# Optimization experiments

Hardware: AMD Instinct MI355X
Metric: run time of the kernel (lower is better)

## Reference

```python
import jax, jax.numpy as jnp
import numpy as np

B, S, D = 64, 2048, 512


def setup_inputs() -> dict:
    key = jax.random.key(0)
    k1, k2, k3, k4 = jax.random.split(key, 4)
    decoder_output = jax.random.normal(k1, (B, 1, D), dtype=jnp.float32)
    encoder_output = jax.random.normal(k2, (B, S, D), dtype=jnp.float32)
    # W_a_tanh: Dense(D) applied to concat([dec, enc]) of width 2D
    scale_w = 1.0 / np.sqrt(2 * D)
    W_t = jax.random.normal(k3, (2 * D, D), dtype=jnp.float32) * scale_w
    b_t = jnp.zeros((D,), dtype=jnp.float32)
    # v_a: Dense(1)
    v_a = jax.random.normal(k4, (D, 1), dtype=jnp.float32) * (1.0 / np.sqrt(D))
    b_v = jnp.zeros((1,), dtype=jnp.float32)
    return {
        "decoder_output": decoder_output,
        "encoder_output": encoder_output,
        "W_t": W_t,
        "b_t": b_t,
        "v_a": v_a,
        "b_v": b_v,
    }


def reference(decoder_output, encoder_output, W_t, b_t, v_a, b_v):
    # concat-variant Luong attention
    dec = jnp.broadcast_to(decoder_output, encoder_output.shape)       # [B,S,D]
    concated = jnp.concatenate((dec, encoder_output), axis=-1)          # [B,S,2D]
    hidden = jnp.tanh(jnp.einsum('bse,ed->bsd', concated, W_t) + b_t)   # [B,S,D]
    score = (jnp.einsum('bsd,do->bso', hidden, v_a) + b_v)              # [B,S,1]
    score = jnp.transpose(score, (0, 2, 1))                             # [B,1,S]
    alignment_vector = jax.nn.softmax(score, axis=2)                    # [B,1,S]
    context_vector = jnp.matmul(alignment_vector, encoder_output)       # [B,1,D]
    return (context_vector, alignment_vector)
```

## Files before the change

kernel.cpp:

```cpp
#include <hip/hip_runtime.h>
#include <hip/hip_bf16.h>

#define BB 64
#define SS 2048
#define DD 512
#define MM (BB * SS)

typedef __attribute__((ext_vector_type(8))) short bf16x8;
typedef __attribute__((ext_vector_type(4))) float f32x4;

__device__ __forceinline__ unsigned f2bf(float f) {
    unsigned u = __float_as_uint(f);
    u += 0x7FFFu + ((u >> 16) & 1u);
    return u >> 16;
}

__device__ __forceinline__ float fast_tanh(float x) {
    float ax = fabsf(x);
    float e = __expf(-2.0f * ax);
    float t = (1.0f - e) * __builtin_amdgcn_rcpf(1.0f + e);
    return x < 0.0f ? -t : t;
}

__global__ void prep_w(const float* __restrict__ W, short* __restrict__ Bt) {
    __shared__ float tile[64][65];
    int kt = blockIdx.x >> 3;
    int nt = blockIdx.x & 7;
    int t = threadIdx.x;
    int c = t & 63;
    int rbase = (t >> 6) * 16;
    #pragma unroll
    for (int i = 0; i < 16; ++i) {
        int r = rbase + i;
        tile[r][c] = W[(size_t)(512 + kt * 64 + r) * DD + nt * 64 + c];
    }
    __syncthreads();
    #pragma unroll
    for (int i = 0; i < 16; ++i) {
        int r = rbase + i;
        Bt[(size_t)(nt * 64 + r) * DD + kt * 64 + c] = (short)f2bf(tile[c][r]);
    }
}

__global__ void prep_p(const float* __restrict__ dec, const float* __restrict__ W,
                       const float* __restrict__ bt, float* __restrict__ p) {
    int b = blockIdx.x;
    int d = blockIdx.y * 256 + threadIdx.x;
    float acc = bt[d];
    const float* dv = dec + (size_t)b * DD;
    #pragma unroll 8
    for (int e = 0; e < DD; ++e)
        acc += dv[e] * W[(size_t)e * DD + d];
    p[(size_t)b * DD + d] = acc;
}

__global__ __launch_bounds__(256, 2)
void score_gemm(const float* __restrict__ enc,
                const short* __restrict__ Bt,
                const float* __restrict__ p,
                const float* __restrict__ va,
                float* __restrict__ score) {
    __shared__ short Alds[2][128 * 32];
    __shared__ short Blds[2][128 * 32];
    __shared__ float sp[4][64];

    const int tid  = threadIdx.x;
    const int wave = tid >> 6;
    const int lane = tid & 63;
    const int mblk = blockIdx.x >> 2;
    const int n0   = (blockIdx.x & 3) * 128;
    const int m0   = mblk * 128;

    const int wm = wave >> 1, wn = wave & 1;
    const int lm = lane & 15, lq = lane >> 4;

    f32x4 acc[4][4];
    #pragma unroll
    for (int i = 0; i < 4; ++i)
        #pragma unroll
        for (int j = 0; j < 4; ++j)
            acc[i][j] = (f32x4){0.f, 0.f, 0.f, 0.f};

    const int arow = tid >> 1;
    const int acol = (tid & 1) * 16;
    const float* aptr = enc + (size_t)(m0 + arow) * DD + acol;

    const short* bptr = Bt + (size_t)(n0 + wave * 32 + (lane >> 2)) * DD + (lane & 3) * 8;

    #pragma unroll
    for (int i = 0; i < 2; ++i)
        __builtin_amdgcn_global_load_lds(
            (const __attribute__((address_space(1))) void*)(bptr + (size_t)i * 16 * DD),
            (__attribute__((address_space(3))) void*)(&Blds[0][(wave * 32 + i * 16) * 32]),
            16, 0, 0);
    {
        f32x4 x0 = *(const f32x4*)(aptr);
        f32x4 x1 = *(const f32x4*)(aptr + 4);
        f32x4 x2 = *(const f32x4*)(aptr + 8);
        f32x4 x3 = *(const f32x4*)(aptr + 12);
        int4 p0, p1;
        p0.x = f2bf(x0.x) | (f2bf(x0.y) << 16);
        p0.y = f2bf(x0.z) | (f2bf(x0.w) << 16);
        p0.z = f2bf(x1.x) | (f2bf(x1.y) << 16);
        p0.w = f2bf(x1.z) | (f2bf(x1.w) << 16);
        p1.x = f2bf(x2.x) | (f2bf(x2.y) << 16);
        p1.y = f2bf(x2.z) | (f2bf(x2.w) << 16);
        p1.z = f2bf(x3.x) | (f2bf(x3.y) << 16);
        p1.w = f2bf(x3.z) | (f2bf(x3.w) << 16);
        *(int4*)(&Alds[0][arow * 32 + acol]) = p0;
        *(int4*)(&Alds[0][arow * 32 + acol + 8]) = p1;
    }
    __syncthreads();

    for (int kt = 0; kt < 16; ++kt) {
        const int c = kt & 1;
        const bool pf = kt < 15;
        f32x4 x0, x1, x2, x3;
        if (pf) {
            const int kn = (kt + 1) * 32;
            #pragma unroll
            for (int i = 0; i < 2; ++i)
                __builtin_amdgcn_global_load_lds(
                    (const __attribute__((address_space(1))) void*)(bptr + (size_t)i * 16 * DD + kn),
                    (__attribute__((address_space(3))) void*)(&Blds[1 - c][(wave * 32 + i * 16) * 32]),
                    16, 0, 0);
            x0 = *(const f32x4*)(aptr + kn);
            x1 = *(const f32x4*)(aptr + kn + 4);
            x2 = *(const f32x4*)(aptr + kn + 8);
            x3 = *(const f32x4*)(aptr + kn + 12);
        }
        bf16x8 af[4];
        #pragma unroll
        for (int mf = 0; mf < 4; ++mf)
            af[mf] = *(const bf16x8*)(&Alds[c][(wm * 64 + mf * 16 + lm) * 32 + lq * 8]);
        #pragma unroll
        for (int nf = 0; nf < 4; ++nf) {
            bf16x8 bfr = *(const bf16x8*)(&Blds[c][(wn * 64 + nf * 16 + lm) * 32 + lq * 8]);
            #pragma unroll
            for (int mf = 0; mf < 4; ++mf)
                acc[mf][nf] = __builtin_amdgcn_mfma_f32_16x16x32_bf16(af[mf], bfr, acc[mf][nf], 0, 0, 0);
        }
        if (pf) {
            int4 p0, p1;
            p0.x = f2bf(x0.x) | (f2bf(x0.y) << 16);
            p0.y = f2bf(x0.z) | (f2bf(x0.w) << 16);
            p0.z = f2bf(x1.x) | (f2bf(x1.y) << 16);
            p0.w = f2bf(x1.z) | (f2bf(x1.w) << 16);
            p1.x = f2bf(x2.x) | (f2bf(x2.y) << 16);
            p1.y = f2bf(x2.z) | (f2bf(x2.w) << 16);
            p1.z = f2bf(x3.x) | (f2bf(x3.y) << 16);
            p1.w = f2bf(x3.z) | (f2bf(x3.w) << 16);
            *(int4*)(&Alds[1 - c][arow * 32 + acol]) = p0;
            *(int4*)(&Alds[1 - c][arow * 32 + acol + 8]) = p1;
        }
        __syncthreads();
    }

    const int b = m0 >> 11;
    float rowsum[4][4];
    #pragma unroll
    for (int mf = 0; mf < 4; ++mf)
        #pragma unroll
        for (int r = 0; r < 4; ++r) rowsum[mf][r] = 0.f;

    #pragma unroll
    for (int nf = 0; nf < 4; ++nf) {
        int n = n0 + wn * 64 + nf * 16 + lm;
        float pv = p[(size_t)b * DD + n];
        float vv = va[n];
        #pragma unroll
        for (int mf = 0; mf < 4; ++mf)
            #pragma unroll
            for (int r = 0; r < 4; ++r)
                rowsum[mf][r] += fast_tanh(pv + acc[mf][nf][r]) * vv;
    }
    #pragma unroll
    for (int mf = 0; mf < 4; ++mf)
        #pragma unroll
        for (int r = 0; r < 4; ++r) {
            float s = rowsum[mf][r];
            s += __shfl_xor(s, 1);
            s += __shfl_xor(s, 2);
            s += __shfl_xor(s, 4);
            s += __shfl_xor(s, 8);
            rowsum[mf][r] = s;
        }
    if (lm == 0) {
        #pragma unroll
        for (int mf = 0; mf < 4; ++mf)
            #pragma unroll
            for (int r = 0; r < 4; ++r)
                sp[wave][mf * 16 + lq * 4 + r] = rowsum[mf][r];
    }
    __syncthreads();
    if (tid < 128) {
        int row = tid & 63, half = tid >> 6;
        float v = sp[half * 2][row] + sp[half * 2 + 1][row];
        atomicAdd(&score[(size_t)m0 + half * 64 + row], v);
    }
}

__global__ void softmax_k(const float* __restrict__ score, float* __restrict__ align) {
    __shared__ float red[256];
    int b = blockIdx.x, tid = threadIdx.x;
    const float* s = score + (size_t)b * SS;
    float vals[8];
    float mx = -1e30f;
    #pragma unroll
    for (int i = 0; i < 8; ++i) {
        vals[i] = s[i * 256 + tid];
        mx = fmaxf(mx, vals[i]);
    }
    red[tid] = mx; __syncthreads();
    for (int off = 128; off > 0; off >>= 1) {
        if (tid < off) red[tid] = fmaxf(red[tid], red[tid + off]);
        __syncthreads();
    }
    mx = red[0]; __syncthreads();
    float sum = 0.f;
    #pragma unroll
    for (int i = 0; i < 8; ++i) {
        vals[i] = __expf(vals[i] - mx);
        sum += vals[i];
    }
    red[tid] = sum; __syncthreads();
    for (int off = 128; off > 0; off >>= 1) {
        if (tid < off) red[tid] += red[tid + off];
        __syncthreads();
    }
    float inv = 1.0f / red[0];
    #pragma unroll
    for (int i = 0; i < 8; ++i)
        align[(size_t)b * SS + i * 256 + tid] = vals[i] * inv;
}

__global__ void context_k(const float* __restrict__ enc, const float* __restrict__ align,
                          float* __restrict__ ctx) {
    int bx = blockIdx.x;
    int b = bx >> 4, chunk = bx & 15;
    int tid = threadIdx.x;
    const float2* e2 = (const float2*)(enc + ((size_t)b * SS + chunk * 128) * DD);
    const float* a = align + (size_t)b * SS + chunk * 128;
    float2 acc = {0.f, 0.f};
    #pragma unroll 4
    for (int s = 0; s < 128; ++s) {
        float av = a[s];
        float2 e = e2[(size_t)s * 256 + tid];
        acc.x += av * e.x;
        acc.y += av * e.y;
    }
    atomicAdd(&ctx[(size_t)b * DD + tid * 2], acc.x);
    atomicAdd(&ctx[(size_t)b * DD + tid * 2 + 1], acc.y);
}

extern "C" void kernel_launch(void* const* d_in, const int* in_sizes, int n_in,
                              void* d_out, int out_size, void* d_ws, size_t ws_size,
                              hipStream_t stream) {
    const float* dec = (const float*)d_in[0];
    const float* enc = (const float*)d_in[1];
    const float* W   = (const float*)d_in[2];
    const float* bt  = (const float*)d_in[3];
    const float* va  = (const float*)d_in[4];

    float* out   = (float*)d_out;
    float* ctx   = out;
    float* align = out + BB * DD;

    char*  ws    = (char*)d_ws;
    short* Bt    = (short*)ws;
    float* p     = (float*)(ws + 512 * 512 * 2);
    float* score = (float*)(ws + 512 * 512 * 2 + BB * DD * 4);

    hipMemsetAsync(ctx, 0, BB * DD * sizeof(float), stream);
    hipMemsetAsync(score, 0, MM * sizeof(float), stream);
    prep_w<<<64, 256, 0, stream>>>(W, Bt);
    prep_p<<<dim3(BB, 2), 256, 0, stream>>>(dec, W, bt, p);
    score_gemm<<<MM / 32, 256, 0, stream>>>(enc, Bt, p, va, score);
    softmax_k<<<BB, 256, 0, stream>>>(score, align);
    context_k<<<BB * 16, 256, 0, stream>>>(enc, align, ctx);
}
```

Before: 538.5 us.

## Fuse score GEMM, local softmax and context into one flash-style kernel

Replaces the separate score GEMM, softmax and context kernels with one fused kernel. Each block keeps a 64-row encoder slab in LDS as a bf16 hi/lo split, computes the scores over the full N=512 with 8 waves, then takes a local max and sum and forms a partial context from the LDS copy. A small combine kernel rescales the partial results into ctx and align. This removes the second read of the encoder from HBM, the score atomics and the memsets. In exchange it uses 128KB of LDS per block, which lowers occupancy, and it reads B fragments straight from global memory instead of staging them in LDS.

```diff
diff --git a/kernel.cpp b/kernel.cpp
--- a/kernel.cpp
+++ b/kernel.cpp
@@ -1,10 +1,8 @@
 #include <hip/hip_runtime.h>
-#include <hip/hip_bf16.h>
 
 #define BB 64
 #define SS 2048
 #define DD 512
-#define MM (BB * SS)
 
 typedef __attribute__((ext_vector_type(8))) short bf16x8;
 typedef __attribute__((ext_vector_type(4))) float f32x4;
@@ -54,25 +52,57 @@
     p[(size_t)b * DD + d] = acc;
 }
 
-__global__ __launch_bounds__(256, 2)
-void score_gemm(const float* __restrict__ enc,
-                const short* __restrict__ Bt,
-                const float* __restrict__ p,
-                const float* __restrict__ va,
-                float* __restrict__ score) {
-    __shared__ short Alds[2][128 * 32];
-    __shared__ short Blds[2][128 * 32];
-    __shared__ float sp[4][64];
+__device__ __forceinline__ void write_slab(char* AhiB, char* AloB, unsigned off, f32x4 x) {
+    unsigned hb0 = f2bf(x.x), hb1 = f2bf(x.y), hb2 = f2bf(x.z), hb3 = f2bf(x.w);
+    uint2 hv;
+    hv.x = hb0 | (hb1 << 16);
+    hv.y = hb2 | (hb3 << 16);
+    float r0 = x.x - __uint_as_float(hb0 << 16);
+    float r1 = x.y - __uint_as_float(hb1 << 16);
+    float r2 = x.z - __uint_as_float(hb2 << 16);
+    float r3 = x.w - __uint_as_float(hb3 << 16);
+    uint2 lv;
+    lv.x = f2bf(r0) | (f2bf(r1) << 16);
+    lv.y = f2bf(r2) | (f2bf(r3) << 16);
+    *(uint2*)(AhiB + off) = hv;
+    *(uint2*)(AloB + off) = lv;
+}
+
+__global__ __launch_bounds__(512, 2)
+void fused_k(const float* __restrict__ enc, const short* __restrict__ Bt,
+             const float* __restrict__ p, const float* __restrict__ va,
+             float* __restrict__ score, float* __restrict__ ml,
+             float* __restrict__ pctx) {
+    __shared__ short Ahi[64 * 512];
+    __shared__ short Alo[64 * 512];
+    __shared__ float sp[8][64];
+    __shared__ float elds[64];
+    __shared__ float sp2[4][512];
 
     const int tid  = threadIdx.x;
     const int wave = tid >> 6;
     const int lane = tid & 63;
-    const int mblk = blockIdx.x >> 2;
-    const int n0   = (blockIdx.x & 3) * 128;
-    const int m0   = mblk * 128;
-
-    const int wm = wave >> 1, wn = wave & 1;
-    const int lm = lane & 15, lq = lane >> 4;
+    const int lm   = lane & 15;
+    const int lq   = lane >> 4;
+    const int blk  = blockIdx.x;
+    const int b    = blk >> 5;
+    const size_t m0 = (size_t)blk * 64;
+
+    char* AhiB = (char*)Ahi;
+    char* AloB = (char*)Alo;
+
+    const int srow = tid >> 3;
+    const int skc8 = (tid & 7) * 8;
+    const unsigned srowB = (unsigned)srow * 1024;
+    const unsigned swsr  = (unsigned)(srow & 7) << 4;
+    const float* aptr = enc + m0 * DD + (size_t)srow * DD + (tid & 7) * 4;
+
+    const unsigned lq16 = (unsigned)lq * 16;
+    const unsigned swlm = (unsigned)(lm & 7) << 4;
+    unsigned arow[4];
+    #pragma unroll
+    for (int mf = 0; mf < 4; ++mf) arow[mf] = (unsigned)(mf * 16 + lm) * 1024;
+    const short* Bw = Bt + (size_t)(wave * 64 + lm) * DD + lq * 8;
 
     f32x4 acc[4][4];
     #pragma unroll
@@ -81,82 +111,35 @@
         for (int j = 0; j < 4; ++j)
             acc[i][j] = (f32x4){0.f, 0.f, 0.f, 0.f};
 
-    const int arow = tid >> 1;
-    const int acol = (tid & 1) * 16;
-    const float* aptr = enc + (size_t)(m0 + arow) * DD + acol;
-
-    const short* bptr = Bt + (size_t)(n0 + wave * 32 + (lane >> 2)) * DD + (lane & 3) * 8;
-
-    #pragma unroll
-    for (int i = 0; i < 2; ++i)
-        __builtin_amdgcn_global_load_lds(
-            (const __attribute__((address_space(1))) void*)(bptr + (size_t)i * 16 * DD),
-            (__attribute__((address_space(3))) void*)(&Blds[0][(wave * 32 + i * 16) * 32]),
-            16, 0, 0);
-    {
-        f32x4 x0 = *(const f32x4*)(aptr);
-        f32x4 x1 = *(const f32x4*)(aptr + 4);
-        f32x4 x2 = *(const f32x4*)(aptr + 8);
-        f32x4 x3 = *(const f32x4*)(aptr + 12);
-        int4 p0, p1;
-        p0.x = f2bf(x0.x) | (f2bf(x0.y) << 16);
-        p0.y = f2bf(x0.z) | (f2bf(x0.w) << 16);
-        p0.z = f2bf(x1.x) | (f2bf(x1.y) << 16);
-        p0.w = f2bf(x1.z) | (f2bf(x1.w) << 16);
-        p1.x = f2bf(x2.x) | (f2bf(x2.y) << 16);
-        p1.y = f2bf(x2.z) | (f2bf(x2.w) << 16);
-        p1.z = f2bf(x3.x) | (f2bf(x3.y) << 16);
-        p1.w = f2bf(x3.z) | (f2bf(x3.w) << 16);
-        *(int4*)(&Alds[0][arow * 32 + acol]) = p0;
-        *(int4*)(&Alds[0][arow * 32 + acol + 8]) = p1;
-    }
-    __syncthreads();
-
+    f32x4 stg[2];
+    stg[0] = *(const f32x4*)(aptr);
+    stg[1] = *(const f32x4*)(aptr + 32);
+    write_slab(AhiB, AloB, srowB + ((unsigned)skc8 ^ swsr), stg[0]);
+    __syncthreads();
+
+    #pragma unroll
     for (int kt = 0; kt < 16; ++kt) {
-        const int c = kt & 1;
-        const bool pf = kt < 15;
-        f32x4 x0, x1, x2, x3;
-        if (pf) {
-            const int kn = (kt + 1) * 32;
-            #pragma unroll
-            for (int i = 0; i < 2; ++i)
-                __builtin_amdgcn_global_load_lds(
-                    (const __attribute__((address_space(1))) void*)(bptr + (size_t)i * 16 * DD + kn),
-                    (__attribute__((address_space(3))) void*)(&Blds[1 - c][(wave * 32 + i * 16) * 32]),
-                    16, 0, 0);
-            x0 = *(const f32x4*)(aptr + kn);
-            x1 = *(const f32x4*)(aptr + kn + 4);
-            x2 = *(const f32x4*)(aptr + kn + 8);
-            x3 = *(const f32x4*)(aptr + kn + 12);
-        }
+        if (kt < 14) stg[kt & 1] = *(const f32x4*)(aptr + (kt + 2) * 32);
+        const unsigned kx = ((unsigned)(kt * 64) + lq16) ^ swlm;
         bf16x8 af[4];
         #pragma unroll
         for (int mf = 0; mf < 4; ++mf)
-            af[mf] = *(const bf16x8*)(&Alds[c][(wm * 64 + mf * 16 + lm) * 32 + lq * 8]);
+            af[mf] = *(const bf16x8*)(AhiB + (arow[mf] + kx));
         #pragma unroll
         for (int nf = 0; nf < 4; ++nf) {
-            bf16x8 bfr = *(const bf16x8*)(&Blds[c][(wn * 64 + nf * 16 + lm) * 32 + lq * 8]);
+            bf16x8 bfr = *(const bf16x8*)(Bw + nf * 16 * DD + kt * 32);
             #pragma unroll
             for (int mf = 0; mf < 4; ++mf)
                 acc[mf][nf] = __builtin_amdgcn_mfma_f32_16x16x32_bf16(af[mf], bfr, acc[mf][nf], 0, 0, 0);
         }
-        if (pf) {
-            int4 p0, p1;
-            p0.x = f2bf(x0.x) | (f2bf(x0.y) << 16);
-            p0.y = f2bf(x0.z) | (f2bf(x0.w) << 16);
-            p0.z = f2bf(x1.x) | (f2bf(x1.y) << 16);
-            p0.w = f2bf(x1.z) | (f2bf(x1.w) << 16);
-            p1.x = f2bf(x2.x) | (f2bf(x2.y) << 16);
-            p1.y = f2bf(x2.z) | (f2bf(x2.w) << 16);
-            p1.z = f2bf(x3.x) | (f2bf(x3.y) << 16);
-            p1.w = f2bf(x3.z) | (f2bf(x3.w) << 16);
-            *(int4*)(&Alds[1 - c][arow * 32 + acol]) = p0;
-            *(int4*)(&Alds[1 - c][arow * 32 + acol + 8]) = p1;
+        if (kt < 15) {
+            unsigned off = srowB + (((unsigned)((kt + 1) * 64 + skc8)) ^ swsr);
+            write_slab(AhiB, AloB, off, stg[(kt + 1) & 1]);
         }
         __syncthreads();
     }
 
-    const int b = m0 >> 11;
+    const float* pb = p + (size_t)b * DD;
     float rowsum[4][4];
     #pragma unroll
     for (int mf = 0; mf < 4; ++mf)
@@ -165,8 +148,8 @@
 
     #pragma unroll
     for (int nf = 0; nf < 4; ++nf) {
-        int n = n0 + wn * 64 + nf * 16 + lm;
-        float pv = p[(size_t)b * DD + n];
+        int n = wave * 64 + nf * 16 + lm;
+        float pv = pb[n];
         float vv = va[n];
         #pragma unroll
         for (int mf = 0; mf < 4; ++mf)
@@ -193,64 +176,92 @@
                 sp[wave][mf * 16 + lq * 4 + r] = rowsum[mf][r];
     }
     __syncthreads();
-    if (tid < 128) {
-        int row = tid & 63, half = tid >> 6;
-        float v = sp[half * 2][row] + sp[half * 2 + 1][row];
-        atomicAdd(&score[(size_t)m0 + half * 64 + row], v);
-    }
-}
-
-__global__ void softmax_k(const float* __restrict__ score, float* __restrict__ align) {
-    __shared__ float red[256];
-    int b = blockIdx.x, tid = threadIdx.x;
-    const float* s = score + (size_t)b * SS;
-    float vals[8];
-    float mx = -1e30f;
+
+    if (tid < 64) {
+        float s = 0.f;
+        #pragma unroll
+        for (int w = 0; w < 8; ++w) s += sp[w][tid];
+        score[m0 + tid] = s;
+        float mx = s;
+        #pragma unroll
+        for (int off = 32; off > 0; off >>= 1) mx = fmaxf(mx, __shfl_xor(mx, off));
+        float e = __expf(s - mx);
+        float l = e;
+        #pragma unroll
+        for (int off = 32; off > 0; off >>= 1) l += __shfl_xor(l, off);
+        elds[tid] = e;
+        if (tid == 0) {
+            ml[(size_t)blk * 2]     = mx;
+            ml[(size_t)blk * 2 + 1] = l;
+        }
+    }
+    __syncthreads();
+
+    {
+        const int q = tid & 127;
+        const int g = tid >> 7;
+        const unsigned dbyte = (unsigned)q * 8;
+        float c0 = 0.f, c1 = 0.f, c2 = 0.f, c3 = 0.f;
+        #pragma unroll
+        for (int si = 0; si < 16; ++si) {
+            int s = g * 16 + si;
+            float ev = elds[s];
+            unsigned off = (unsigned)s * 1024 + (dbyte ^ ((unsigned)(s & 7) << 4));
+            uint2 hv = *(const uint2*)(AhiB + off);
+            uint2 lv = *(const uint2*)(AloB + off);
+            c0 += ev * (__uint_as_float(hv.x << 16) + __uint_as_float(lv.x << 16));
+            c1 += ev * (__uint_as_float(hv.x & 0xffff0000u) + __uint_as_float(lv.x & 0xffff0000u));
+            c2 += ev * (__uint_as_float(hv.y << 16) + __uint_as_float(lv.y << 16));
+            c3 += ev * (__uint_as_float(hv.y & 0xffff0000u) + __uint_as_float(lv.y & 0xffff0000u));
+        }
+        *(f32x4*)(&sp2[g][q * 4]) = (f32x4){c0, c1, c2, c3};
+    }
+    __syncthreads();
+    {
+        float v = sp2[0][tid] + sp2[1][tid] + sp2[2][tid] + sp2[3][tid];
+        pctx[(size_t)blk * 512 + tid] = v;
+    }
+}
+
+__global__ void combine_k(const float* __restrict__ score, const float* __restrict__ ml,
+                          const float* __restrict__ pctx, float* __restrict__ ctx,
+                          float* __restrict__ align) {
+    __shared__ float sc[32];
+    __shared__ float MB, LB;
+    const int b = blockIdx.x, tid = threadIdx.x;
+    if (tid < 32) sc[tid] = ml[(size_t)(b * 32 + tid) * 2];
+    __syncthreads();
+    if (tid == 0) {
+        float M = sc[0];
+        #pragma unroll
+        for (int i = 1; i < 32; ++i) M = fmaxf(M, sc[i]);
+        float L = 0.f;
+        for (int i = 0; i < 32; ++i) {
+            float w = __expf(sc[i] - M);
+            L += w * ml[(size_t)(b * 32 + i) * 2 + 1];
+            sc[i] = w;
+        }
+        MB = M;
+        LB = L;
+    }
+    __syncthreads();
+    const float M = MB, Linv = 1.0f / LB;
+    float a0 = 0.f, a1 = 0.f;
+    for (int i = 0; i < 32; ++i) {
+        float w = sc[i];
+        const float* pc = pctx + (size_t)(b * 32 + i) * 512;
+        a0 += w * pc[tid];
+        a1 += w * pc[tid + 256];
+    }
+    ctx[(size_t)b * DD + tid]       = a0 * Linv;
+    ctx[(size_t)b * DD + tid + 256] = a1 * Linv;
+    const float* sr = score + (size_t)b * SS;
+    float* al = align + (size_t)b * SS;
     #pragma unroll
     for (int i = 0; i < 8; ++i) {
-        vals[i] = s[i * 256 + tid];
-        mx = fmaxf(mx, vals[i]);
-    }
-    red[tid] = mx; __syncthreads();
-    for (int off = 128; off > 0; off >>= 1) {
-        if (tid < off) red[tid] = fmaxf(red[tid], red[tid + off]);
-        __syncthreads();
-    }
-    mx = red[0]; __syncthreads();
-    float sum = 0.f;
-    #pragma unroll
-    for (int i = 0; i < 8; ++i) {
-        vals[i] = __expf(vals[i] - mx);
-        sum += vals[i];
-    }
-    red[tid] = sum; __syncthreads();
-    for (int off = 128; off > 0; off >>= 1) {
-        if (tid < off) red[tid] += red[tid + off];
-        __syncthreads();
-    }
-    float inv = 1.0f / red[0];
-    #pragma unroll
-    for (int i = 0; i < 8; ++i)
-        align[(size_t)b * SS + i * 256 + tid] = vals[i] * inv;
-}
-
-__global__ void context_k(const float* __restrict__ enc, const float* __restrict__ align,
-                          float* __restrict__ ctx) {
-    int bx = blockIdx.x;
-    int b = bx >> 4, chunk = bx & 15;
-    int tid = threadIdx.x;
-    const float2* e2 = (const float2*)(enc + ((size_t)b * SS + chunk * 128) * DD);
-    const float* a = align + (size_t)b * SS + chunk * 128;
-    float2 acc = {0.f, 0.f};
-    #pragma unroll 4
-    for (int s = 0; s < 128; ++s) {
-        float av = a[s];
-        float2 e = e2[(size_t)s * 256 + tid];
-        acc.x += av * e.x;
-        acc.y += av * e.y;
-    }
-    atomicAdd(&ctx[(size_t)b * DD + tid * 2], acc.x);
-    atomicAdd(&ctx[(size_t)b * DD + tid * 2 + 1], acc.y);
+        int s = i * 256 + tid;
+        al[s] = __expf(sr[s] - M) * Linv;
+    }
 }
 
 extern "C" void kernel_launch(void* const* d_in, const int* in_sizes, int n_in,
@@ -268,14 +279,13 @@
 
     char*  ws    = (char*)d_ws;
     short* Bt    = (short*)ws;
-    float* p     = (float*)(ws + 512 * 512 * 2);
-    float* score = (float*)(ws + 512 * 512 * 2 + BB * DD * 4);
-
-    hipMemsetAsync(ctx, 0, BB * DD * sizeof(float), stream);
-    hipMemsetAsync(score, 0, MM * sizeof(float), stream);
+    float* p     = (float*)(ws + 524288);
+    float* score = (float*)(ws + 655360);
+    float* ml    = (float*)(ws + 1179648);
+    float* pctx  = (float*)(ws + 1196032);
+
     prep_w<<<64, 256, 0, stream>>>(W, Bt);
     prep_p<<<dim3(BB, 2), 256, 0, stream>>>(dec, W, bt, p);
-    score_gemm<<<MM / 32, 256, 0, stream>>>(enc, Bt, p, va, score);
-    softmax_k<<<BB, 256, 0, stream>>>(score, align);
-    context_k<<<BB * 16, 256, 0, stream>>>(enc, align, ctx);
-}
+    fused_k<<<BB * 32, 512, 0, stream>>>(enc, Bt, p, va, score, ml, pctx);
+    combine_k<<<BB, 256, 0, stream>>>(score, ml, pctx, ctx, align);
+}
```

Result: slower. 554.8 us (+3.0%).
